# Performance work log

Hardware: AMD Instinct MI355X
Metric: run time of the kernel (lower is better)

Reference implementation:

```python
import jax, jax.numpy as jnp
import numpy as np


def setup_inputs() -> dict:
    key = jax.random.key(0)
    k1, k2 = jax.random.split(key)
    B, N, M, D = 8, 8192, 8192, 3
    input1 = jax.random.normal(k1, (B, N, D), dtype=jnp.float32)
    input2 = jax.random.normal(k2, (B, M, D), dtype=jnp.float32)
    return {"input1": input1, "input2": input2}


def reference(input1, input2):
    # input1: [B, N, 3], input2: [B, M, 3]
    # Squared pairwise distances via ||x||^2 + ||y||^2 - 2<x,y>
    sq1 = jnp.sum(input1 * input1, axis=-1)          # [B, N]
    sq2 = jnp.sum(input2 * input2, axis=-1)          # [B, M]
    inner = jnp.einsum('bnd,bmd->bnm', input1, input2)  # [B, N, M]
    d = sq1[:, :, None] + sq2[:, None, :] - 2.0 * inner  # [B, N, M]
    d = jnp.maximum(d, 0.0)  # numerical guard
    dist1 = jnp.min(d, axis=2)  # [B, N] NN in input2 for each point of input1
    dist2 = jnp.min(d, axis=1)  # [B, M] NN in input1 for each point of input2
    loss = jnp.mean(dist1) + jnp.mean(dist2)
    return loss
```

## Files before the change

### kernel.cpp

```cpp
#include <hip/hip_runtime.h>


typedef _Float16 half8 __attribute__((ext_vector_type(8)));
typedef float    f16x  __attribute__((ext_vector_type(16)));

constexpr int B      = 8;
constexpr int NPTS   = 8192;
constexpr int TOTAL  = B * NPTS;
constexpr int NSTRIP = 256;
constexpr int MHALF  = 4096;
constexpr int CHUNK  = 512;

__device__ __forceinline__ float colmin16(const f16x& a)
{
    float m0 = fminf(fminf(a[0],  a[1]),  a[2]);
    float m1 = fminf(fminf(a[3],  a[4]),  a[5]);
    float m2 = fminf(fminf(a[6],  a[7]),  a[8]);
    float m3 = fminf(fminf(a[9],  a[10]), a[11]);
    float m4 = fminf(fminf(a[12], a[13]), a[14]);
    return fminf(fminf(fminf(m0, m1), m2), fminf(fminf(m3, m4), a[15]));
}

__global__ __launch_bounds__(512, 4) void chamfer_mfma(
    const float* __restrict__ in1, const float* __restrict__ in2,
    float* __restrict__ d1p, float* __restrict__ d2p, float* __restrict__ out)
{
    const int b     = blockIdx.z;
    const int strip = blockIdx.x;
    const int mh    = blockIdx.y;
    const int wave  = threadIdx.x >> 6;
    const int lane  = threadIdx.x & 63;
    const int col   = lane & 31;
    const int half  = lane >> 5;

    if ((blockIdx.x | blockIdx.y | blockIdx.z) == 0 && threadIdx.x == 0)
        *out = 0.0f;

    __shared__ _Float16 ldsB[CHUNK * 16];
    __shared__ unsigned d2lds[MHALF];

    for (int i = threadIdx.x; i < MHALF; i += 512)
        d2lds[i] = 0xFFFFFFFFu;

    const int nbase = strip * NSTRIP + wave * 32;
    half8 afrag;
    {
        const float* a = in1 + ((size_t)b * NPTS + nbase + col) * 3;
        float x = a[0], y = a[1], z = a[2];
        float sq = fmaf(x, x, fmaf(y, y, z * z));
        _Float16 xh = (_Float16)x, yh = (_Float16)y, zh = (_Float16)z;
        _Float16 xl = (_Float16)(x - (float)xh);
        _Float16 yl = (_Float16)(y - (float)yh);
        _Float16 zl = (_Float16)(z - (float)zh);
        _Float16 sh = (_Float16)sq, sl = (_Float16)(sq - (float)sh);
        half8 lo = {xh, yh, zh, xl, yl, zl, xh, yh};
        half8 hi = {zh, sh, sl, (_Float16)1.f, (_Float16)1.f,
                    (_Float16)0.f, (_Float16)0.f, (_Float16)0.f};
        afrag = half ? hi : lo;
    }

    f16x MN1, zero;
#pragma unroll
    for (int r = 0; r < 16; ++r) { MN1[r] = 1e30f; zero[r] = 0.0f; }

    const float* Craw = in2 + ((size_t)b * NPTS + mh * MHALF) * 3;

    for (int c = 0; c < MHALF / CHUNK; ++c) {
        __syncthreads();
        {
            const float* cp = Craw + (size_t)(c * CHUNK + threadIdx.x) * 3;
            float cx = cp[0], cy = cp[1], cz = cp[2];
            float x = -2.f * cx, y = -2.f * cy, z = -2.f * cz;
            float sq = fmaf(cx, cx, fmaf(cy, cy, cz * cz));
            _Float16 xh = (_Float16)x, yh = (_Float16)y, zh = (_Float16)z;
            _Float16 xl = (_Float16)(x - (float)xh);
            _Float16 yl = (_Float16)(y - (float)yh);
            _Float16 zl = (_Float16)(z - (float)zh);
            _Float16 sh = (_Float16)sq, sl = (_Float16)(sq - (float)sh);
            half8 lo = {xh, yh, zh, xh, yh, zh, xl, yl};
            half8 hi = {zl, (_Float16)1.f, (_Float16)1.f, sh, sl,
                        (_Float16)0.f, (_Float16)0.f, (_Float16)0.f};
            *(half8*)&ldsB[threadIdx.x * 16]     = lo;
            *(half8*)&ldsB[threadIdx.x * 16 + 8] = hi;
        }
        __syncthreads();

#pragma unroll 2
        for (int t = 0; t < CHUNK / 32; t += 2) {
            half8 bfA = *(const half8*)&ldsB[((t    ) * 32 + col) * 16 + half * 8];
            half8 bfB = *(const half8*)&ldsB[((t + 1) * 32 + col) * 16 + half * 8];
            f16x accA = __builtin_amdgcn_mfma_f32_32x32x16_f16(afrag, bfA, zero, 0, 0, 0);
            f16x accB = __builtin_amdgcn_mfma_f32_32x32x16_f16(afrag, bfB, zero, 0, 0, 0);

#pragma unroll
            for (int r = 0; r < 16; ++r)
                MN1[r] = fminf(fminf(MN1[r], accA[r]), accB[r]);

            float vA = fmaxf(colmin16(accA), 0.0f);
            atomicMin(&d2lds[c * CHUNK + t * 32 + col], __float_as_uint(vA));
            float vB = fmaxf(colmin16(accB), 0.0f);
            atomicMin(&d2lds[c * CHUNK + (t + 1) * 32 + col], __float_as_uint(vB));
        }
    }
    __syncthreads();

    float* d2 = d2p + ((size_t)b * 32 + strip) * NPTS + mh * MHALF;
    for (int i = threadIdx.x; i < MHALF; i += 512)
        d2[i] = __uint_as_float(d2lds[i]);

#pragma unroll
    for (int m = 1; m <= 16; m <<= 1)
#pragma unroll
        for (int r = 0; r < 16; ++r)
            MN1[r] = fminf(MN1[r], __shfl_xor(MN1[r], m, 64));
    if (col == 0) {
        float* d1 = d1p + ((size_t)b * 2 + mh) * NPTS + nbase;
#pragma unroll
        for (int r = 0; r < 16; ++r)
            d1[(r & 3) + 8 * (r >> 2) + 4 * half] = MN1[r];
    }
}

__global__ __launch_bounds__(256) void reduce_kernel(
    const float* __restrict__ d1p, const float* __restrict__ d2p,
    float* __restrict__ out)
{
    int g  = blockIdx.x * 256 + threadIdx.x;
    int b  = g >> 11;
    int mq = g & 2047;

    const float4* p2 = (const float4*)(d2p + (size_t)b * 32 * NPTS) + mq;
    float4 v2 = p2[0];
#pragma unroll
    for (int s = 1; s < 32; ++s) {
        float4 t = p2[(size_t)s * (NPTS / 4)];
        v2.x = fminf(v2.x, t.x); v2.y = fminf(v2.y, t.y);
        v2.z = fminf(v2.z, t.z); v2.w = fminf(v2.w, t.w);
    }
    float4 a0 = ((const float4*)(d1p + ((size_t)b * 2 + 0) * NPTS))[mq];
    float4 a1 = ((const float4*)(d1p + ((size_t)b * 2 + 1) * NPTS))[mq];
    float v = fmaxf(fminf(a0.x, a1.x), 0.0f) + fmaxf(fminf(a0.y, a1.y), 0.0f)
            + fmaxf(fminf(a0.z, a1.z), 0.0f) + fmaxf(fminf(a0.w, a1.w), 0.0f)
            + v2.x + v2.y + v2.z + v2.w;

#pragma unroll
    for (int off = 32; off; off >>= 1)
        v += __shfl_down(v, off, 64);
    __shared__ float wsum[4];
    int lane = threadIdx.x & 63, w = threadIdx.x >> 6;
    if (lane == 0) wsum[w] = v;
    __syncthreads();
    if (threadIdx.x == 0)
        atomicAdd(out, (wsum[0] + wsum[1] + wsum[2] + wsum[3]) *
                           (1.0f / (float)TOTAL));
}

extern "C" void kernel_launch(void* const* d_in, const int* in_sizes, int n_in,
                              void* d_out, int out_size, void* d_ws, size_t ws_size,
                              hipStream_t stream)
{
    const float* in1 = (const float*)d_in[0];
    const float* in2 = (const float*)d_in[1];
    float* out = (float*)d_out;

    char* ws = (char*)d_ws;
    float* d1p = (float*)ws;
    float* d2p = (float*)(ws + (size_t)2 * TOTAL * 4);

    chamfer_mfma<<<dim3(NPTS / NSTRIP, 2, B), 512, 0, stream>>>(
        in1, in2, d1p, d2p, out);
    reduce_kernel<<<TOTAL / 1024, 256, 0, stream>>>(d1p, d2p, out);
}
```

Measured before the change: 92.13 us.

## Halve block size, prefetch next B chunk into registers, split LDS lo/hi

Blocks now have 256 threads (4 waves, 128 rows per strip), which doubles the number of strips and of d2 partial rows the reduce kernel must combine. Each thread packs two B points per chunk, and the next chunk's global load and f16 packing are issued after the barrier so they overlap the MFMA loop. The LDS B buffer is split into separate lo and hi arrays to change the read stride. The cost is twice as many d2 partial writes and reduce reads, and each block re-initialises the 4096-entry d2 LDS array for half as much compute.

After: 100.0 us. 1.09x slower.

```diff
diff --git a/kernel.cpp b/kernel.cpp
--- a/kernel.cpp
+++ b/kernel.cpp
@@ -7,9 +7,11 @@
 constexpr int B      = 8;
 constexpr int NPTS   = 8192;
 constexpr int TOTAL  = B * NPTS;
-constexpr int NSTRIP = 256;
+constexpr int NSTRIP = 128;
+constexpr int NSTR   = NPTS / NSTRIP;
 constexpr int MHALF  = 4096;
 constexpr int CHUNK  = 512;
+constexpr int NCHUNK = MHALF / CHUNK;
 
 __device__ __forceinline__ float colmin16(const f16x& a)
 {
@@ -21,7 +23,23 @@
     return fminf(fminf(fminf(m0, m1), m2), fminf(fminf(m3, m4), a[15]));
 }
 
-__global__ __launch_bounds__(512, 4) void chamfer_mfma(
+__device__ __forceinline__ void pack_b(const float* __restrict__ cp,
+                                       half8& lo, half8& hi)
+{
+    float cx = cp[0], cy = cp[1], cz = cp[2];
+    float x = -2.f * cx, y = -2.f * cy, z = -2.f * cz;
+    float sq = fmaf(cx, cx, fmaf(cy, cy, cz * cz));
+    _Float16 xh = (_Float16)x, yh = (_Float16)y, zh = (_Float16)z;
+    _Float16 xl = (_Float16)(x - (float)xh);
+    _Float16 yl = (_Float16)(y - (float)yh);
+    _Float16 zl = (_Float16)(z - (float)zh);
+    _Float16 sh = (_Float16)sq, sl = (_Float16)(sq - (float)sh);
+    lo = half8{xh, yh, zh, xh, yh, zh, xl, yl};
+    hi = half8{zl, (_Float16)1.f, (_Float16)1.f, sh, sl,
+               (_Float16)0.f, (_Float16)0.f, (_Float16)0.f};
+}
+
+__global__ __launch_bounds__(256, 4) void chamfer_mfma(
     const float* __restrict__ in1, const float* __restrict__ in2,
     float* __restrict__ d1p, float* __restrict__ d2p, float* __restrict__ out)
 {
@@ -36,10 +54,11 @@
     if ((blockIdx.x | blockIdx.y | blockIdx.z) == 0 && threadIdx.x == 0)
         *out = 0.0f;
 
-    __shared__ _Float16 ldsB[CHUNK * 16];
+    __shared__ _Float16 ldsLo[CHUNK * 8];
+    __shared__ _Float16 ldsHi[CHUNK * 8];
     __shared__ unsigned d2lds[MHALF];
 
-    for (int i = threadIdx.x; i < MHALF; i += 512)
+    for (int i = threadIdx.x; i < MHALF; i += 256)
         d2lds[i] = 0xFFFFFFFFu;
 
     const int nbase = strip * NSTRIP + wave * 32;
@@ -65,30 +84,29 @@
 
     const float* Craw = in2 + ((size_t)b * NPTS + mh * MHALF) * 3;
 
-    for (int c = 0; c < MHALF / CHUNK; ++c) {
+    half8 lo0, hi0, lo1, hi1;
+    pack_b(Craw + (size_t)threadIdx.x * 3,         lo0, hi0);
+    pack_b(Craw + (size_t)(threadIdx.x + 256) * 3, lo1, hi1);
+
+    for (int c = 0; c < NCHUNK; ++c) {
         __syncthreads();
-        {
-            const float* cp = Craw + (size_t)(c * CHUNK + threadIdx.x) * 3;
-            float cx = cp[0], cy = cp[1], cz = cp[2];
-            float x = -2.f * cx, y = -2.f * cy, z = -2.f * cz;
-            float sq = fmaf(cx, cx, fmaf(cy, cy, cz * cz));
-            _Float16 xh = (_Float16)x, yh = (_Float16)y, zh = (_Float16)z;
-            _Float16 xl = (_Float16)(x - (float)xh);
-            _Float16 yl = (_Float16)(y - (float)yh);
-            _Float16 zl = (_Float16)(z - (float)zh);
-            _Float16 sh = (_Float16)sq, sl = (_Float16)(sq - (float)sh);
-            half8 lo = {xh, yh, zh, xh, yh, zh, xl, yl};
-            half8 hi = {zl, (_Float16)1.f, (_Float16)1.f, sh, sl,
-                        (_Float16)0.f, (_Float16)0.f, (_Float16)0.f};
-            *(half8*)&ldsB[threadIdx.x * 16]     = lo;
-            *(half8*)&ldsB[threadIdx.x * 16 + 8] = hi;
-        }
+        *(half8*)&ldsLo[threadIdx.x * 8]         = lo0;
+        *(half8*)&ldsHi[threadIdx.x * 8]         = hi0;
+        *(half8*)&ldsLo[(threadIdx.x + 256) * 8] = lo1;
+        *(half8*)&ldsHi[(threadIdx.x + 256) * 8] = hi1;
         __syncthreads();
 
+        if (c + 1 < NCHUNK) {
+            const float* n0 = Craw + (size_t)((c + 1) * CHUNK + threadIdx.x) * 3;
+            pack_b(n0,                  lo0, hi0);
+            pack_b(n0 + 256 * 3,        lo1, hi1);
+        }
+
+        const _Float16* fragBase = half ? ldsHi : ldsLo;
 #pragma unroll 2
         for (int t = 0; t < CHUNK / 32; t += 2) {
-            half8 bfA = *(const half8*)&ldsB[((t    ) * 32 + col) * 16 + half * 8];
-            half8 bfB = *(const half8*)&ldsB[((t + 1) * 32 + col) * 16 + half * 8];
+            half8 bfA = *(const half8*)&fragBase[((t    ) * 32 + col) * 8];
+            half8 bfB = *(const half8*)&fragBase[((t + 1) * 32 + col) * 8];
             f16x accA = __builtin_amdgcn_mfma_f32_32x32x16_f16(afrag, bfA, zero, 0, 0, 0);
             f16x accB = __builtin_amdgcn_mfma_f32_32x32x16_f16(afrag, bfB, zero, 0, 0, 0);
 
@@ -104,8 +122,8 @@
     }
     __syncthreads();
 
-    float* d2 = d2p + ((size_t)b * 32 + strip) * NPTS + mh * MHALF;
-    for (int i = threadIdx.x; i < MHALF; i += 512)
+    float* d2 = d2p + ((size_t)b * NSTR + strip) * NPTS + mh * MHALF;
+    for (int i = threadIdx.x; i < MHALF; i += 256)
         d2[i] = __uint_as_float(d2lds[i]);
 
 #pragma unroll
@@ -129,10 +147,10 @@
     int b  = g >> 11;
     int mq = g & 2047;
 
-    const float4* p2 = (const float4*)(d2p + (size_t)b * 32 * NPTS) + mq;
+    const float4* p2 = (const float4*)(d2p + (size_t)b * NSTR * NPTS) + mq;
     float4 v2 = p2[0];
 #pragma unroll
-    for (int s = 1; s < 32; ++s) {
+    for (int s = 1; s < NSTR; ++s) {
         float4 t = p2[(size_t)s * (NPTS / 4)];
         v2.x = fminf(v2.x, t.x); v2.y = fminf(v2.y, t.y);
         v2.z = fminf(v2.z, t.z); v2.w = fminf(v2.w, t.w);
@@ -167,7 +185,7 @@
     float* d1p = (float*)ws;
     float* d2p = (float*)(ws + (size_t)2 * TOTAL * 4);
 
-    chamfer_mfma<<<dim3(NPTS / NSTRIP, 2, B), 512, 0, stream>>>(
+    chamfer_mfma<<<dim3(NPTS / NSTRIP, 2, B), 256, 0, stream>>>(
         in1, in2, d1p, d2p, out);
     reduce_kernel<<<TOTAL / 1024, 256, 0, stream>>>(d1p, d2p, out);
 }
```
